# Kernel tuning notes

Measured on AMD Instinct MI355X. Metric: run time of the kernel, lower is better.

The kernel has to match this reference:

```python
import jax, jax.numpy as jnp
import numpy as np

LOG_SCALE_INIT = float(np.log(10.0))


def lorentz_linear(x, W, b, log_scale):
    # nonlin (gelu) -> linear -> Lorentz time/space renormalization
    y = jax.nn.gelu(x) @ W.T + b
    time = jax.nn.sigmoid(y[..., :1]) * jnp.exp(log_scale) + 1.1
    nar = y[..., 1:]
    denom = jnp.clip(jnp.sum(nar * nar, axis=-1, keepdims=True), 1e-8, None)
    scale = (time * time - 1.0) / denom
    return jnp.concatenate([time, nar * jnp.sqrt(scale)], axis=-1)


def ffn_lorentz(x, W1, b1, s1, W2, b2, s2):
    return lorentz_linear(lorentz_linear(x, W1, b1, s1), W2, b2, s2) + x


def knn_indices(x, k):
    # x: (B,N,C). KNN on detached features (as in ViG dense_knn_matrix).
    xs = jax.lax.stop_gradient(x)
    sq = jnp.sum(xs * xs, axis=-1)  # (B,N)
    d = sq[:, :, None] + sq[:, None, :] - 2.0 * jnp.einsum('bnc,bmc->bnm', xs, xs)
    _, idx = jax.lax.top_k(-d, k)  # (B,N,k) nearest (includes self)
    return idx


def graph_conv(x, Wg, bg, sg, k):
    # Max-relative graph conv with Lorentz linear. x: (B,N,C)
    idx = knn_indices(x, k)
    xj = jax.vmap(lambda xb, ib: xb[ib])(x, idx)  # (B,N,k,C) gather
    msg = jnp.max(xj - x[:, :, None, :], axis=2)  # (B,N,C)
    h = jnp.concatenate([x, msg], axis=-1)        # (B,N,2C)
    return lorentz_linear(h, Wg, bg, sg)


def setup_inputs() -> dict:
    key = jax.random.key(0)
    ks = jax.random.split(key, 8)
    B, C, H, W = 8, 192, 56, 56
    x = jax.random.normal(ks[0], (B, C, H, W), dtype=jnp.float32)
    def lin(k_, fin, fout):
        return jax.random.normal(k_, (fout, fin), dtype=jnp.float32) * 0.02
    p = {
        'x': x,
        'W1': lin(ks[1], C, C), 'b1': jnp.zeros((C,), jnp.float32), 's1': jnp.float32(LOG_SCALE_INIT),
        'W2': lin(ks[2], C, C), 'b2': jnp.zeros((C,), jnp.float32), 's2': jnp.float32(LOG_SCALE_INIT),
        'Wg': lin(ks[3], 2 * C, C), 'bg': jnp.zeros((C,), jnp.float32), 'sg': jnp.float32(LOG_SCALE_INIT),
        'W3': lin(ks[4], C, C), 'b3': jnp.zeros((C,), jnp.float32), 's3': jnp.float32(LOG_SCALE_INIT),
        'W4': lin(ks[5], C, C), 'b4': jnp.zeros((C,), jnp.float32), 's4': jnp.float32(LOG_SCALE_INIT),
        'k': 9,
    }
    return p


def reference(x, W1, b1, s1, W2, b2, s2, Wg, bg, sg, W3, b3, s3, W4, b4, s4, k):
    B, C, H, W = x.shape
    xn = x.reshape(B, C, H * W).transpose(0, 2, 1)  # (B,N,C) == rearrange b c (h w) 1 -> b (h w) c
    shortcut = xn
    xn = ffn_lorentz(xn, W1, b1, s1, W2, b2, s2)
    xn = graph_conv(xn, Wg, bg, sg, k)
    xn = ffn_lorentz(xn, W3, b3, s3, W4, b4, s4)
    xn = xn + shortcut  # drop_path = 0 -> identity
    return xn.transpose(0, 2, 1).reshape(B, C, H, W)
```

## Files before the change

kernel.cpp:

```cpp
#include <hip/hip_runtime.h>
#include <math.h>

#define NB   8
#define NC   192
#define NPIX 3136
#define NPAD 3200
#define NMT  98
#define GRID_LL (NB*NMT)
#define NIT  25
#define NSP  8
#define GRID_KNN (NB*NIT*NSP)
#define GRID_MSG (NB*196)
#define FINF 3.4e38f

typedef _Float16 f16x8 __attribute__((ext_vector_type(8)));
typedef float   f32x16 __attribute__((ext_vector_type(16)));

__device__ __forceinline__ float gelu_f(float x){
    float u = 0.7978845608028654f * (x + 0.044715f * x * x * x);
    return 0.5f * x * (1.0f + tanhf(u));
}
__device__ __forceinline__ unsigned short h2u(_Float16 v){
    union { _Float16 f; unsigned short u; } c; c.f = v; return c.u;
}
__device__ __forceinline__ unsigned pack_hi(float a, float b){
    return (unsigned)h2u((_Float16)a) | ((unsigned)h2u((_Float16)b) << 16);
}

#define LESS9(da,ia,db,ib) ((da) < (db) || ((da) == (db) && (ia) < (ib)))
#define CSW9(a,ia,b,ib) { bool sw_ = LESS9(b,ib,a,ia); float tf_=(a); int ti_=(ia); \
    (a) = sw_? (b) : (a); (ia) = sw_? (ib) : (ia); (b) = sw_? tf_ : (b); (ib) = sw_? ti_ : (ib); }

struct Top9 {
    float d0,d1,d2,d3,d4,d5,d6,d7,d8;
    int   j0,j1,j2,j3,j4,j5,j6,j7,j8;
    __device__ __forceinline__ void init(){
        d0=d1=d2=d3=d4=d5=d6=d7=d8=FINF;
        j0=j1=j2=j3=j4=j5=j6=j7=j8=0x7FFFFFFF;
    }
    __device__ __forceinline__ void insert(float nd, int ni){
        if (!LESS9(nd, ni, d8, j8)) return;
        d8 = nd; j8 = ni;
        CSW9(d7,j7,d8,j8); CSW9(d6,j6,d7,j7); CSW9(d5,j5,d6,j6); CSW9(d4,j4,d5,j5);
        CSW9(d3,j3,d4,j4); CSW9(d2,j2,d3,j3); CSW9(d1,j1,d2,j2); CSW9(d0,j0,d1,j1);
    }
};

__device__ __forceinline__ unsigned f2mono(float e){
    unsigned u = __float_as_uint(e);
    return u ^ ((unsigned)((int)u >> 31) | 0x80000000u);
}
__device__ __forceinline__ float unmono(unsigned m){
    return __uint_as_float(m ^ ((unsigned)(((int)~m) >> 31) | 0x80000000u));
}

#define CSK(a,b) { unsigned h_ = (a) > (b) ? (a) : (b); unsigned l_ = (a) > (b) ? (b) : (a); (a) = h_; (b) = l_; }
#define INSKEY(x_) if ((x_) > t_k11){ t_k11 = (x_); \
    CSK(t_k10,t_k11) CSK(t_k9,t_k10) CSK(t_k8,t_k9) CSK(t_k7,t_k8) \
    CSK(t_k6,t_k7) CSK(t_k5,t_k6) CSK(t_k4,t_k5) CSK(t_k3,t_k4) \
    CSK(t_k2,t_k3) CSK(t_k1,t_k2) CSK(t_k0,t_k1) }

#define KQ(A,Q) { \
    unsigned q0_ = (f2mono(A[4*(Q)+0]) & 0xFFFFF000u) | (unsigned)(jinvb_ - 8*(Q)    ); \
    unsigned q1_ = (f2mono(A[4*(Q)+1]) & 0xFFFFF000u) | (unsigned)(jinvb_ - 8*(Q) - 1); \
    unsigned q2_ = (f2mono(A[4*(Q)+2]) & 0xFFFFF000u) | (unsigned)(jinvb_ - 8*(Q) - 2); \
    unsigned q3_ = (f2mono(A[4*(Q)+3]) & 0xFFFFF000u) | (unsigned)(jinvb_ - 8*(Q) - 3); \
    unsigned qa_ = q0_ > q1_ ? q0_ : q1_; \
    unsigned qb_ = q2_ > q3_ ? q2_ : q3_; \
    unsigned qm_ = qa_ > qb_ ? qa_ : qb_; \
    if (qm_ > t_k11){ INSKEY(q0_) INSKEY(q1_) INSKEY(q2_) INSKEY(q3_) } }

#define AMAX16(A) fmaxf(fmaxf(fmaxf(fmaxf(A[0],A[1]),fmaxf(A[2],A[3])),fmaxf(fmaxf(A[4],A[5]),fmaxf(A[6],A[7]))), \
                        fmaxf(fmaxf(fmaxf(A[8],A[9]),fmaxf(A[10],A[11])),fmaxf(fmaxf(A[12],A[13]),fmaxf(A[14],A[15]))))

#define INSACCK(A,JS) { float am_ = AMAX16(A); \
    if (am_ >= thrf){ int jinvb_ = 4095 - (jg + (JS)*32 + 4*h); \
        KQ(A,0) KQ(A,1) KQ(A,2) KQ(A,3) } }

#define MF(ACC,AO,BO) ACC = __builtin_amdgcn_mfma_f32_32x32x16_f16(AO,BO,ACC,0,0,0);
#define ZERO16 {0,0,0,0,0,0,0,0,0,0,0,0,0,0,0,0}

__global__ __launch_bounds__(256) void wt_kernel(
    const float* __restrict__ W1, const float* __restrict__ W2,
    float* __restrict__ W1T, float* __restrict__ W2T)
{
    __shared__ float tile[32*33];
    int t = blockIdx.x;
    const float* src; float* dst;
    if (t < 36){ src = W1; dst = W1T; } else { src = W2; dst = W2T; t -= 36; }
    int tr = t / 6, tc = t - tr*6;
    int tid = threadIdx.x;
    {
        int i = tid >> 3, j4 = (tid & 7)*4;
        float4 v = *(const float4*)&src[(size_t)(tr*32 + i)*192 + tc*32 + j4];
        tile[i*33 + j4+0] = v.x; tile[i*33 + j4+1] = v.y;
        tile[i*33 + j4+2] = v.z; tile[i*33 + j4+3] = v.w;
    }
    __syncthreads();
    {
        int j = tid >> 3, i4 = (tid & 7)*4;
        float4 o = make_float4(tile[(i4+0)*33 + j], tile[(i4+1)*33 + j],
                               tile[(i4+2)*33 + j], tile[(i4+3)*33 + j]);
        *(float4*)&dst[(size_t)(tc*32 + j)*192 + tr*32 + i4] = o;
    }
}

__global__ __launch_bounds__(256) void wt16_kernel(
    const float* __restrict__ Wg, const float* __restrict__ W3,
    const float* __restrict__ W4,
    unsigned short* __restrict__ Wh, unsigned short* __restrict__ Wl)
{
    int i = blockIdx.x*256 + threadIdx.x;
    if (i >= 147456) return;
    const float* src; int off;
    if (i < 73728)       { src = Wg; off = i; }
    else if (i < 110592) { src = W3; off = i - 73728; }
    else                 { src = W4; off = i - 110592; }
    float w = src[off];
    _Float16 hi = (_Float16)w;
    Wh[i] = h2u(hi);
    Wl[i] = h2u((_Float16)(w - (float)hi));
}

__global__ __launch_bounds__(256) void pad_kernel(
    unsigned short* __restrict__ Xh, unsigned short* __restrict__ S2h)
{
    const int b = blockIdx.x;
    const int tid = threadIdx.x;
    uint4 z = make_uint4(0,0,0,0);
    for (int e = tid; e < 1536; e += 256){
        int r = e / 24, c8 = (e % 24) * 8;
        *(uint4*)&Xh[((size_t)b*NPAD + NPIX + r)*192 + c8] = z;
    }
    if (tid < 64){
        union { _Float16 f; unsigned short u; } p;
        p.f = (_Float16)(-30000.0f);
        S2h[(size_t)b*NPAD + NPIX + tid] = p.u;
    }
}

template<int K, bool WCM, bool DUAL, bool AX, bool CONVF>
__global__ __launch_bounds__(256, 4) void ll2_kernel(
    const float* __restrict__ A0, const float* __restrict__ A1,
    const float* __restrict__ WT, const float* __restrict__ bias,
    const float* __restrict__ sptr, const float* __restrict__ Xres,
    float* __restrict__ OutCM, float* __restrict__ Hrm,
    unsigned short* __restrict__ Xh, unsigned short* __restrict__ S2h,
    float* __restrict__ SQf)
{
    __shared__ float lA[32*36];
    __shared__ float lW[32*196];

    const int tid = threadIdx.x;
    const int tx = tid & 15, ty = tid >> 4;
    const int bid = blockIdx.x;
    const int b  = bid / NMT;
    const int n0 = (bid % NMT) * 32;

    float acc[2][12];
    #pragma unroll
    for (int mi = 0; mi < 2; ++mi)
        #pragma unroll
        for (int j = 0; j < 12; ++j) acc[mi][j] = 0.f;

    for (int kt = 0; kt < K/32; ++kt){
        {
            int kk = tid >> 3;
            int m4 = (tid & 7) * 4;
            int c  = kt*32 + kk;
            const float* pl;
            if (K > 192 && c >= 192) pl = A1 + ((size_t)b*192 + (c - 192))*NPIX;
            else                     pl = A0 + ((size_t)b*192 + c)*NPIX;
            float4 v = *(const float4*)&pl[n0 + m4];
            v.x = gelu_f(v.x); v.y = gelu_f(v.y); v.z = gelu_f(v.z); v.w = gelu_f(v.w);
            *(float4*)&lA[kk*36 + m4] = v;
        }
        #pragma unroll
        for (int r = 0; r < 6; ++r){
            int e  = tid + r*256;
            int kk = e / 48;
            int c4 = (e - kk*48) * 4;
            float4 v = *(const float4*)&WT[(size_t)(kt*32 + kk)*192 + c4];
            *(float4*)&lW[kk*196 + c4] = v;
        }
        __syncthreads();
        #pragma unroll
        for (int kk = 0; kk < 32; ++kk){
            float2 a2 = *(const float2*)&lA[kk*36 + ty*2];
            float4 w0 = *(const float4*)&lW[kk*196 + tx*12];
            float4 w1 = *(const float4*)&lW[kk*196 + tx*12 + 4];
            float4 w2 = *(const float4*)&lW[kk*196 + tx*12 + 8];
            float aw[2]  = {a2.x, a2.y};
            float wv[12] = {w0.x,w0.y,w0.z,w0.w, w1.x,w1.y,w1.z,w1.w, w2.x,w2.y,w2.z,w2.w};
            #pragma unroll
            for (int mi = 0; mi < 2; ++mi)
                #pragma unroll
                for (int j = 0; j < 12; ++j)
                    acc[mi][j] = fmaf(aw[mi], wv[j], acc[mi][j]);
        }
        __syncthreads();
    }

    const int lane = tid & 63;
    float es = expf(sptr[0]);
    float bv[12];
    #pragma unroll
    for (int q = 0; q < 3; ++q){
        float4 t4 = *(const float4*)&bias[tx*12 + q*4];
        bv[q*4+0] = t4.x; bv[q*4+1] = t4.y; bv[q*4+2] = t4.z; bv[q*4+3] = t4.w;
    }
    #pragma unroll
    for (int mi = 0; mi < 2; ++mi){
        float part = 0.f;
        #pragma unroll
        for (int j = 0; j < 12; ++j){
            float y = acc[mi][j] + bv[j];
            acc[mi][j] = y;
            if (!(tx == 0 && j == 0)) part += y * y;
        }
        #pragma unroll
        for (int m = 1; m < 16; m <<= 1) part += __shfl_xor(part, m, 64);
        float y0   = __shfl(acc[mi][0], lane & 48, 64);
        float tval = es / (1.f + expf(-y0)) + 1.1f;
        float denom = fmaxf(part, 1e-8f);
        float sca  = (tval*tval - 1.f) / denom;
        float sqs  = sqrtf(sca);
        #pragma unroll
        for (int j = 0; j < 12; ++j){
            float o = acc[mi][j] * sqs;
            if (tx == 0 && j == 0) o = tval;
            acc[mi][j] = o;
        }
    }
    if (AX){
        #pragma unroll
        for (int j = 0; j < 12; ++j){
            int c = tx*12 + j;
            float2 xv = *(const float2*)&Xres[((size_t)b*192 + c)*NPIX + n0 + ty*2];
            acc[0][j] += xv.x; acc[1][j] += xv.y;
        }
    }
    if (WCM){
        #pragma unroll
        for (int j = 0; j < 12; ++j){
            int c = tx*12 + j;
            *(float2*)&OutCM[((size_t)b*192 + c)*NPIX + n0 + ty*2] = make_float2(acc[0][j], acc[1][j]);
        }
    }
    if (DUAL){
        #pragma unroll
        for (int mi = 0; mi < 2; ++mi){
            #pragma unroll
            for (int q = 0; q < 3; ++q){
                float4 o = make_float4(acc[mi][q*4+0], acc[mi][q*4+1], acc[mi][q*4+2], acc[mi][q*4+3]);
                *(float4*)&Hrm[((size_t)b*NPIX + n0 + ty*2 + mi)*192 + tx*12 + q*4] = o;
            }
        }
    }
    if (CONVF){
        #pragma unroll
        for (int mi = 0; mi < 2; ++mi){
            int row = n0 + ty*2 + mi;
            float s = 0.f;
            #pragma unroll
            for (int j = 0; j < 12; ++j) s = fmaf(acc[mi][j], acc[mi][j], s);
            #pragma unroll
            for (int m = 1; m < 16; m <<= 1) s += __shfl_xor(s, m, 64);
            #pragma unroll
            for (int q = 0; q < 3; ++q){
                uint2 hv;
                hv.x = pack_hi(acc[mi][q*4+0], acc[mi][q*4+1]);
                hv.y = pack_hi(acc[mi][q*4+2], acc[mi][q*4+3]);
                *(uint2*)&Xh[((size_t)b*NPAD + row)*192 + tx*12 + q*4] = hv;
            }
            if (tx == 0){
                SQf[(size_t)b*NPIX + row] = s;
                S2h[(size_t)b*NPAD + row] = h2u((_Float16)(-0.5f * s));
            }
        }
    }
}

template<int K, int AMODE, bool ESPL, bool EF32, bool AXCM, bool ARRM, bool OUTCM>
__global__ __launch_bounds__(192) void mll_kernel(
    const unsigned short* __restrict__ Ash, const unsigned short* __restrict__ Asl,
    const float* __restrict__ Af0, const float* __restrict__ Af1,
    const unsigned short* __restrict__ Wh, const unsigned short* __restrict__ Wl,
    const float* __restrict__ bias, const float* __restrict__ sptr,
    const float* __restrict__ Xcm, const float* __restrict__ Rrm,
    float* __restrict__ OutF,
    unsigned short* __restrict__ Oh, unsigned short* __restrict__ Ol)
{
    __shared__ float psum[3][32], y0v[32];
    const int tid = threadIdx.x;
    const int w = tid >> 6, lane = tid & 63, l31 = lane & 31, h = lane >> 5;
    const int bid = blockIdx.x;
    const int b = bid / NMT, mt = bid % NMT;
    const int row0 = mt*32;
    const int nb = w*64;
    const size_t arow = (size_t)b*NPIX + row0 + l31;
    const int c0 = nb + l31, c1 = nb + 32 + l31;

    f32x16 acc0 = ZERO16, acc1 = ZERO16;

    #pragma unroll
    for (int ks = 0; ks < K/16; ++ks){
        const int kb = ks*16 + h*8;
        f16x8 ah, al;
        if (AMODE == 0){
            ah = __builtin_bit_cast(f16x8, *(const uint4*)&Ash[arow*192 + kb]);
            al = __builtin_bit_cast(f16x8, *(const uint4*)&Asl[arow*192 + kb]);
        } else {
            const float* src;
            if (AMODE == 2) src = (ks < 12) ? (Af0 + arow*192 + kb) : (Af1 + arow*192 + (kb - 192));
            else            src = Af0 + arow*192 + kb;
            float4 f0 = *(const float4*)src;
            float4 f1 = *(const float4*)(src + 4);
            float g[8] = {f0.x,f0.y,f0.z,f0.w,f1.x,f1.y,f1.z,f1.w};
            #pragma unroll
            for (int e = 0; e < 8; ++e){
                float gg = gelu_f(g[e]);
                _Float16 hi = (_Float16)gg;
                ah[e] = hi;
                al[e] = (_Float16)(gg - (float)hi);
            }
        }
        f16x8 wh0 = __builtin_bit_cast(f16x8, *(const uint4*)&Wh[(size_t)c0*K + kb]);
        f16x8 wl0 = __builtin_bit_cast(f16x8, *(const uint4*)&Wl[(size_t)c0*K + kb]);
        f16x8 wh1 = __builtin_bit_cast(f16x8, *(const uint4*)&Wh[(size_t)c1*K + kb]);
        f16x8 wl1 = __builtin_bit_cast(f16x8, *(const uint4*)&Wl[(size_t)c1*K + kb]);
        MF(acc0, ah, wh0) MF(acc0, al, wh0) MF(acc0, ah, wl0)
        MF(acc1, ah, wh1) MF(acc1, al, wh1) MF(acc1, ah, wl1)
    }

    const float es = expf(sptr[0]);
    const float bv0 = bias[c0], bv1 = bias[c1];
    float o0[16], o1[16], p[16];
    #pragma unroll
    for (int r = 0; r < 16; ++r){
        o0[r] = acc0[r] + bv0;
        o1[r] = acc1[r] + bv1;
        p[r] = o0[r]*o0[r] + o1[r]*o1[r];
    }
    #pragma unroll
    for (int m = 1; m < 32; m <<= 1){
        #pragma unroll
        for (int r = 0; r < 16; ++r) p[r] += __shfl_xor(p[r], m, 64);
    }
    if (l31 == 0){
        #pragma unroll
        for (int r = 0; r < 16; ++r){
            int row = (r&3) + 8*(r>>2) + 4*h;
            float v = p[r];
            if (w == 0){ v -= o0[r]*o0[r]; y0v[row] = o0[r]; }
            psum[w][row] = v;
        }
    }
    __syncthreads();
    #pragma unroll
    for (int r = 0; r < 16; ++r){
        int row = (r&3) + 8*(r>>2) + 4*h;
        float S = psum[0][row] + psum[1][row] + psum[2][row];
        float y0 = y0v[row];
        float tval = es / (1.f + expf(-y0)) + 1.1f;
        float denom = fmaxf(S, 1e-8f);
        float sqs = sqrtf((tval*tval - 1.f)/denom);
        o0[r] *= sqs; o1[r] *= sqs;
        if (w == 0 && l31 == 0) o0[r] = tval;
    }
    if (AXCM){
        #pragma unroll
        for (int p4 = 0; p4 < 4; ++p4){
            float4 xv0 = *(const float4*)&Xcm[((size_t)b*192 + c0)*NPIX + row0 + 8*p4 + 4*h];
            float4 xv1 = *(const float4*)&Xcm[((size_t)b*192 + c1)*NPIX + row0 + 8*p4 + 4*h];
            o0[4*p4+0] += xv0.x; o0[4*p4+1] += xv0.y; o0[4*p4+2] += xv0.z; o0[4*p4+3] += xv0.w;
            o1[4*p4+0] += xv1.x; o1[4*p4+1] += xv1.y; o1[4*p4+2] += xv1.z; o1[4*p4+3] += xv1.w;
        }
    }
    if (ARRM){
        #pragma unroll
        for (int r = 0; r < 16; ++r){
            int row = (r&3) + 8*(r>>2) + 4*h;
            o0[r] += Rrm[((size_t)b*NPIX + row0 + row)*192 + c0];
            o1[r] += Rrm[((size_t)b*NPIX + row0 + row)*192 + c1];
        }
    }
    if (OUTCM){
        #pragma unroll
        for (int p4 = 0; p4 < 4; ++p4){
            *(float4*)&OutF[((size_t)b*192 + c0)*NPIX + row0 + 8*p4 + 4*h] =
                make_float4(o0[4*p4+0], o0[4*p4+1], o0[4*p4+2], o0[4*p4+3]);
            *(float4*)&OutF[((size_t)b*192 + c1)*NPIX + row0 + 8*p4 + 4*h] =
                make_float4(o1[4*p4+0], o1[4*p4+1], o1[4*p4+2], o1[4*p4+3]);
        }
    }
    if (EF32){
        #pragma unroll
        for (int r = 0; r < 16; ++r){
            int row = (r&3) + 8*(r>>2) + 4*h;
            OutF[((size_t)b*NPIX + row0 + row)*192 + c0] = o0[r];
            OutF[((size_t)b*NPIX + row0 + row)*192 + c1] = o1[r];
        }
    }
    if (ESPL){
        #pragma unroll
        for (int r = 0; r < 16; ++r){
            int row = (r&3) + 8*(r>>2) + 4*h;
            size_t o = ((size_t)b*NPIX + row0 + row)*192;
            float g0 = gelu_f(o0[r]);
            _Float16 h0 = (_Float16)g0;
            Oh[o + c0] = h2u(h0);
            Ol[o + c0] = h2u((_Float16)(g0 - (float)h0));
            float g1 = gelu_f(o1[r]);
            _Float16 h1 = (_Float16)g1;
            Oh[o + c1] = h2u(h1);
            Ol[o + c1] = h2u((_Float16)(g1 - (float)h1));
        }
    }
}

__global__ __launch_bounds__(256) __attribute__((amdgpu_waves_per_eu(2))) void knn_kernel(
    const unsigned short* __restrict__ Xh, const unsigned short* __restrict__ S2h,
    unsigned* __restrict__ PK)
{
    __shared__ uint4 lds[1280];

    const int tid  = threadIdx.x;
    const int lane = tid & 63;
    const int w    = tid >> 6;
    const int l31  = lane & 31;
    const int h    = lane >> 5;
    const int bid  = blockIdx.x;
    const int b    = bid & 7;
    const int t2   = bid >> 3;
    const int itile = t2 >> 3;
    const int sp    = t2 & 7;
    const int i0    = itile * 128;
    const int g0 = (sp*25)/NSP, g1 = ((sp+1)*25)/NSP;
    const size_t rowb = (size_t)b * NPAD;

    unsigned t_k0=0,t_k1=0,t_k2=0,t_k3=0,t_k4=0,t_k5=0,
             t_k6=0,t_k7=0,t_k8=0,t_k9=0,t_k10=0,t_k11=0;
    float thrf = -FINF;

    for (int g = g0; g < g1; ++g){
        const int jg = g*128;
        f32x16 acc0 = ZERO16, acc1 = ZERO16, acc2 = ZERO16, acc3 = ZERO16;

        for (int kc = 0; kc < 6; ++kc){
            __syncthreads();
            #pragma unroll
            for (int rr = 0; rr < 4; ++rr){
                int u   = tid + rr*256;
                int arr = u >> 9;
                int rs  = (u >> 2) & 127;
                int seg = u & 3;
                int row = (arr == 0) ? (jg + rs) : (i0 + rs);
                uint4 v = *(const uint4*)&Xh[(rowb + row)*192 + kc*32 + seg*8];
                lds[arr*640 + rs*5 + seg] = v;
            }
            __syncthreads();
            #pragma unroll
            for (int ks = 0; ks < 2; ++ks){
                int kq  = ks*2 + h;
                int rb  = l31*5 + kq;
                f16x8 bh = __builtin_bit_cast(f16x8, lds[640 + w*160 + rb]);
                f16x8 a0h = __builtin_bit_cast(f16x8, lds[  0 + rb]);
                f16x8 a1h = __builtin_bit_cast(f16x8, lds[160 + rb]);
                f16x8 a2h = __builtin_bit_cast(f16x8, lds[320 + rb]);
                f16x8 a3h = __builtin_bit_cast(f16x8, lds[480 + rb]);
                MF(acc0, a0h, bh)
                MF(acc1, a1h, bh)
                MF(acc2, a2h, bh)
                MF(acc3, a3h, bh)
            }
        }

        {
            unsigned m  = (h == 0) ? 0xFFFFFFFFu : 0u;
            unsigned om = 0x3C00u & m;
            f16x8 one = __builtin_bit_cast(f16x8, make_uint4(om, 0, 0, 0));
            unsigned s0 = (unsigned)S2h[rowb + jg +  0 + l31];
            unsigned s1 = (unsigned)S2h[rowb + jg + 32 + l31];
            unsigned s2 = (unsigned)S2h[rowb + jg + 64 + l31];
            unsigned s3 = (unsigned)S2h[rowb + jg + 96 + l31];
            f16x8 a;
            a = __builtin_bit_cast(f16x8, make_uint4(s0 & m, 0,0,0)); MF(acc0, a, one)
            a = __builtin_bit_cast(f16x8, make_uint4(s1 & m, 0,0,0)); MF(acc1, a, one)
            a = __builtin_bit_cast(f16x8, make_uint4(s2 & m, 0,0,0)); MF(acc2, a, one)
            a = __builtin_bit_cast(f16x8, make_uint4(s3 & m, 0,0,0)); MF(acc3, a, one)
        }

        INSACCK(acc0, 0)
        INSACCK(acc1, 1)
        INSACCK(acc2, 2)
        INSACCK(acc3, 3)
        thrf = (t_k11 != 0u) ? unmono(t_k11 & 0xFFFFF000u) : -FINF;
    }

    #define MRGK(Kk) { unsigned ok_ = __shfl((int)(Kk), lane ^ 32, 64); \
                      if (lane < 32) { INSKEY((unsigned)ok_) } }
    MRGK(t_k0) MRGK(t_k1) MRGK(t_k2) MRGK(t_k3) MRGK(t_k4) MRGK(t_k5)
    MRGK(t_k6) MRGK(t_k7) MRGK(t_k8) MRGK(t_k9) MRGK(t_k10) MRGK(t_k11)

    if (lane < 32){
        size_t po = ((size_t)(t2*8 + b)*128 + (size_t)w*32 + l31)*12;
        PK[po+ 0] = t_k0;  PK[po+ 1] = t_k1;  PK[po+ 2] = t_k2;  PK[po+ 3] = t_k3;
        PK[po+ 4] = t_k4;  PK[po+ 5] = t_k5;  PK[po+ 6] = t_k6;  PK[po+ 7] = t_k7;
        PK[po+ 8] = t_k8;  PK[po+ 9] = t_k9;  PK[po+10] = t_k10; PK[po+11] = t_k11;
    }
}

__global__ __launch_bounds__(256) void merge_msg_kernel(
    const float* __restrict__ H, const float* __restrict__ SQf,
    const unsigned* __restrict__ PK, float* __restrict__ Msg)
{
    __shared__ float liX[16*196];
    __shared__ unsigned kv[1600];
    __shared__ float cd[256];
    __shared__ int   cidx[256];
    __shared__ int   fidx[144];

    const int tid = threadIdx.x;
    const int bid = blockIdx.x;
    const int b  = bid / 196;
    const int i0 = (bid % 196) * 16;
    const int base = b * NPIX;

    #pragma unroll
    for (int k = 0; k < 3; ++k){
        int f = tid + k*256;
        int r = f / 48, c4 = f % 48;
        *(float4*)&liX[r*196 + c4*4] = *(const float4*)&H[(size_t)(base + i0 + r)*192 + c4*4];
    }
    if (tid < 128){
        int r = tid >> 3, sp = tid & 7;
        int i = i0 + r;
        size_t po = ((size_t)(((i>>7)*NSP + sp)*8 + b)*128 + (i & 127))*12;
        #pragma unroll
        for (int q = 0; q < 3; ++q)
            *(uint4*)&kv[r*100 + sp*12 + q*4] = *(const uint4*)&PK[po + q*4];
    }
    __syncthreads();

    if (tid < 16){
        int r = tid;
        int h0=0,h1=0,h2=0,h3=0,h4=0,h5=0,h6=0,h7=0;
        #pragma unroll
        for (int p = 0; p < 16; ++p){
            unsigned bk = 0; int bs = 0;
#define HEADC(SP,HV) { \
            unsigned k_ = (HV < 12) ? kv[r*100 + SP*12 + HV] : 0u; \
            bool bt_ = k_ > bk; \
            bk = bt_? k_ : bk; bs = bt_? SP : bs; }
            HEADC(0,h0) HEADC(1,h1) HEADC(2,h2) HEADC(3,h3)
            HEADC(4,h4) HEADC(5,h5) HEADC(6,h6) HEADC(7,h7)
#undef HEADC
            cidx[r*16 + p] = 4095 - (int)(bk & 0xFFFu);
            h0 += (bs==0); h1 += (bs==1); h2 += (bs==2); h3 += (bs==3);
            h4 += (bs==4); h5 += (bs==5); h6 += (bs==6); h7 += (bs==7);
        }
    }
    __syncthreads();

    {
        int r = tid >> 4, p = tid & 15;
        int j = cidx[r*16 + p];
        const float* hj = &H[(size_t)(base + j)*192];
        float dot = 0.f;
        #pragma unroll
        for (int q = 0; q < 48; ++q){
            float4 xv = *(const float4*)&liX[r*196 + q*4];
            float4 yv = *(const float4*)&hj[q*4];
            dot = fmaf(xv.x,yv.x, fmaf(xv.y,yv.y, fmaf(xv.z,yv.z, fmaf(xv.w,yv.w, dot))));
        }
        cd[r*16 + p] = SQf[base + j] - 2.f*dot;
    }
    __syncthreads();

    if (tid < 16){
        int r = tid;
        Top9 m; m.init();
        #pragma unroll
        for (int c = 0; c < 16; ++c) m.insert(cd[r*16 + c], cidx[r*16 + c]);
        fidx[r*9+0]=m.j0; fidx[r*9+1]=m.j1; fidx[r*9+2]=m.j2; fidx[r*9+3]=m.j3;
        fidx[r*9+4]=m.j4; fidx[r*9+5]=m.j5; fidx[r*9+6]=m.j6; fidx[r*9+7]=m.j7;
        fidx[r*9+8]=m.j8;
    }
    __syncthreads();

    int rr = tid >> 4, part = tid & 15;
    int ii = i0 + rr;
    int nbr[9];
    #pragma unroll
    for (int e = 0; e < 9; ++e) nbr[e] = fidx[rr*9 + e];
    #pragma unroll
    for (int q = 0; q < 3; ++q){
        float4 mv = make_float4(-FINF, -FINF, -FINF, -FINF);
        #pragma unroll
        for (int e = 0; e < 9; ++e){
            float4 v = *(const float4*)&H[(size_t)(base + nbr[e])*192 + part*12 + q*4];
            mv.x = fmaxf(mv.x, v.x); mv.y = fmaxf(mv.y, v.y);
            mv.z = fmaxf(mv.z, v.z); mv.w = fmaxf(mv.w, v.w);
        }
        float4 xi = *(const float4*)&liX[rr*196 + part*12 + q*4];
        *(float4*)&Msg[(size_t)(base + ii)*192 + part*12 + q*4] =
            make_float4(mv.x - xi.x, mv.y - xi.y, mv.z - xi.z, mv.w - xi.w);
    }
}

extern "C" void kernel_launch(void* const* d_in, const int* in_sizes, int n_in,
                              void* d_out, int out_size, void* d_ws, size_t ws_size,
                              hipStream_t stream)
{
    const float* x  = (const float*)d_in[0];
    const float* W1 = (const float*)d_in[1];
    const float* b1 = (const float*)d_in[2];
    const float* s1 = (const float*)d_in[3];
    const float* W2 = (const float*)d_in[4];
    const float* b2 = (const float*)d_in[5];
    const float* s2 = (const float*)d_in[6];
    const float* Wg = (const float*)d_in[7];
    const float* bg = (const float*)d_in[8];
    const float* sg = (const float*)d_in[9];
    const float* W3 = (const float*)d_in[10];
    const float* b3 = (const float*)d_in[11];
    const float* s3 = (const float*)d_in[12];
    const float* W4 = (const float*)d_in[13];
    const float* b4 = (const float*)d_in[14];
    const float* s4 = (const float*)d_in[15];
    float* ws = (float*)d_ws;
    float* out = (float*)d_out;

    const size_t NE = (size_t)NB*NPIX*192;
    float* T1cm = ws;
    float* Msg  = ws;
    float* Hrm = ws + NE;
    unsigned short* GT3h = (unsigned short*)Hrm;
    unsigned short* GT3l = GT3h + NE;
    float* X2f = ws + 2*NE;
    unsigned short* Xh  = (unsigned short*)(ws + 3*NE);
    unsigned short* S2h = Xh + (size_t)NB*NPAD*192;
    float* SQf = (float*)(S2h + (size_t)NB*NPAD);
    unsigned* PK = (unsigned*)(SQf + (size_t)NB*NPIX);
    float* W1T = (float*)(PK + (size_t)GRID_KNN*128*12);
    float* W2T = W1T + 36864;
    unsigned short* Wh16 = (unsigned short*)(W2T + 36864);
    unsigned short* Wl16 = Wh16 + 147456;
    const unsigned short* Wgh = Wh16,          *Wgl = Wl16;
    const unsigned short* W3h = Wh16 + 73728,  *W3l = Wl16 + 73728;
    const unsigned short* W4h = Wh16 + 110592, *W4l = Wl16 + 110592;

    wt_kernel<<<72, 256, 0, stream>>>(W1, W2, W1T, W2T);
    wt16_kernel<<<576, 256, 0, stream>>>(Wg, W3, W4, Wh16, Wl16);
    pad_kernel<<<NB, 256, 0, stream>>>(Xh, S2h);
    ll2_kernel<192, true , false, false, false><<<GRID_LL, 256, 0, stream>>>(
        x, x, W1T, b1, s1, nullptr, T1cm, nullptr, nullptr, nullptr, nullptr);
    ll2_kernel<192, false, true , true , true ><<<GRID_LL, 256, 0, stream>>>(
        T1cm, T1cm, W2T, b2, s2, x, nullptr, Hrm, Xh, S2h, SQf);
    knn_kernel<<<GRID_KNN, 256, 0, stream>>>(Xh, S2h, PK);
    merge_msg_kernel<<<GRID_MSG, 256, 0, stream>>>(Hrm, SQf, PK, Msg);
    mll_kernel<384,2,false,true ,false,false,false><<<GRID_LL, 192, 0, stream>>>(
        nullptr, nullptr, Hrm, Msg, Wgh, Wgl, bg, sg, nullptr, nullptr,
        X2f, nullptr, nullptr);
    mll_kernel<192,1,true ,false,false,false,false><<<GRID_LL, 192, 0, stream>>>(
        nullptr, nullptr, X2f, nullptr, W3h, W3l, b3, s3, nullptr, nullptr,
        nullptr, GT3h, GT3l);
    mll_kernel<192,0,false,false,true ,true ,true ><<<GRID_LL, 192, 0, stream>>>(
        GT3h, GT3l, nullptr, nullptr, W4h, W4l, b4, s4, x, X2f,
        out, nullptr, nullptr);
}
```

Baseline: 447.6 us.

## Keep KNN query tile in registers and prefetch next key chunk

The KNN kernel now loads each wave's 32 query rows (all 192 channels) into registers once, instead of restaging the i-tile through shared memory on every k-chunk. This halves shared memory use and the per-chunk global loads. The next j-chunk's global load is issued into registers right after the barrier, so it overlaps with the MFMA work (software prefetch). The cost is higher register pressure (12 f16x8 vectors plus the prefetch buffers), which could hurt occupancy given the waves_per_eu(2) hint.

```diff
diff --git a/kernel.cpp b/kernel.cpp
--- a/kernel.cpp
+++ b/kernel.cpp
@@ -423,7 +423,7 @@
     const unsigned short* __restrict__ Xh, const unsigned short* __restrict__ S2h,
     unsigned* __restrict__ PK)
 {
-    __shared__ uint4 lds[1280];
+    __shared__ uint4 lds[640];
 
     const int tid  = threadIdx.x;
     const int lane = tid & 63;
@@ -439,32 +439,45 @@
     const int g0 = (sp*25)/NSP, g1 = ((sp+1)*25)/NSP;
     const size_t rowb = (size_t)b * NPAD;
 
+    const size_t bbase = (rowb + i0 + w*32 + l31)*192;
+    f16x8 B[6][2];
+    #pragma unroll
+    for (int kc = 0; kc < 6; ++kc)
+        #pragma unroll
+        for (int ks = 0; ks < 2; ++ks)
+            B[kc][ks] = __builtin_bit_cast(f16x8, *(const uint4*)&Xh[bbase + kc*32 + (ks*2 + h)*8]);
+
     unsigned t_k0=0,t_k1=0,t_k2=0,t_k3=0,t_k4=0,t_k5=0,
              t_k6=0,t_k7=0,t_k8=0,t_k9=0,t_k10=0,t_k11=0;
     float thrf = -FINF;
 
+    const int rs0 = tid >> 2, seg0 = tid & 3;
+
+    uint4 pv0 = *(const uint4*)&Xh[(rowb + g0*128 + rs0)*192 + seg0*8];
+    uint4 pv1 = *(const uint4*)&Xh[(rowb + g0*128 + rs0 + 64)*192 + seg0*8];
+
     for (int g = g0; g < g1; ++g){
         const int jg = g*128;
         f32x16 acc0 = ZERO16, acc1 = ZERO16, acc2 = ZERO16, acc3 = ZERO16;
 
+        #pragma unroll
         for (int kc = 0; kc < 6; ++kc){
             __syncthreads();
-            #pragma unroll
-            for (int rr = 0; rr < 4; ++rr){
-                int u   = tid + rr*256;
-                int arr = u >> 9;
-                int rs  = (u >> 2) & 127;
-                int seg = u & 3;
-                int row = (arr == 0) ? (jg + rs) : (i0 + rs);
-                uint4 v = *(const uint4*)&Xh[(rowb + row)*192 + kc*32 + seg*8];
-                lds[arr*640 + rs*5 + seg] = v;
+            lds[rs0*5 + seg0] = pv0;
+            lds[(rs0 + 64)*5 + seg0] = pv1;
+            __syncthreads();
+            {
+                int nkc = (kc < 5) ? kc + 1 : 0;
+                int njg = (kc < 5) ? jg : jg + 128;
+                if (kc < 5 || g + 1 < g1){
+                    pv0 = *(const uint4*)&Xh[(rowb + njg + rs0)*192 + nkc*32 + seg0*8];
+                    pv1 = *(const uint4*)&Xh[(rowb + njg + rs0 + 64)*192 + nkc*32 + seg0*8];
+                }
             }
-            __syncthreads();
             #pragma unroll
             for (int ks = 0; ks < 2; ++ks){
-                int kq  = ks*2 + h;
-                int rb  = l31*5 + kq;
-                f16x8 bh = __builtin_bit_cast(f16x8, lds[640 + w*160 + rb]);
+                int rb = l31*5 + (ks*2 + h);
+                f16x8 bh = B[kc][ks];
                 f16x8 a0h = __builtin_bit_cast(f16x8, lds[  0 + rb]);
                 f16x8 a1h = __builtin_bit_cast(f16x8, lds[160 + rb]);
                 f16x8 a2h = __builtin_bit_cast(f16x8, lds[320 + rb]);
```

Result: faster. 427.9 us (-4.4%).
